# Optimization experiments

Measured on AMD Instinct MI355X. Metric: run time of the kernel, lower is better.

Reference implementation:

```python
import jax, jax.numpy as jnp
import numpy as np

N, F_IN, F_OUT = 8192, 512, 256
ALPHA = 0.2          # LeakyReLU negative slope
NEG_BIG = -9e15      # mask value from the original module


def setup_inputs() -> dict:
    key = jax.random.key(0)
    k1, k2, k3, k4, k5 = jax.random.split(key, 5)
    x = jax.random.normal(k1, (N, F_IN), dtype=jnp.float32)
    adj = jax.random.randint(k2, (N, N), 0, 2, dtype=jnp.int32)
    # xavier_uniform with gain=1.414
    def xavier(k, shape, gain=1.414):
        fan_in, fan_out = shape[0], shape[1]
        bound = gain * np.sqrt(6.0 / (fan_in + fan_out))
        return jax.random.uniform(k, shape, jnp.float32, -bound, bound)
    W = xavier(k3, (F_IN, F_OUT))
    a1 = xavier(k4, (F_OUT, 1))
    a2 = xavier(k5, (F_OUT, 1))
    return {"x": x, "adj": adj, "W": W, "a1": a1, "a2": a2}


def reference(x, adj, W, a1, a2):
    h = x @ W                                   # [N, F_OUT]
    logit_1 = h @ a1                            # [N, 1]
    logit_2 = h @ a2                            # [N, 1]
    e = jax.nn.leaky_relu(logit_1 + logit_2.T, ALPHA)      # [N, N]
    e = jnp.where(adj > 0, e, jnp.float32(NEG_BIG))
    mean_h = jnp.mean(h, axis=0, keepdims=True)            # [1, F_OUT]
    glob_logit = jax.nn.leaky_relu(logit_1 + mean_h @ a2, ALPHA)  # [N, 1]
    e_all = jnp.concatenate([e, glob_logit], axis=-1)      # [N, N+1]
    attention = jax.nn.softmax(e_all, axis=-1)
    h_all = jnp.concatenate([h, mean_h], axis=0)           # [N+1, F_OUT]
    return jax.nn.elu(attention @ h_all)                   # [N, F_OUT]
```

## Files before the change

### kernel.cpp

```cpp
#include <hip/hip_runtime.h>

#define NROW 8192
#define FIN  512
#define FOUT 256
#define ALPHA 0.2f

typedef float  f32x4  __attribute__((ext_vector_type(4)));
typedef int    i32x4  __attribute__((ext_vector_type(4)));
typedef __bf16 bf16x8 __attribute__((ext_vector_type(8)));
typedef __bf16 bf16x4 __attribute__((ext_vector_type(4)));

__device__ __forceinline__ void bar_lds() {
    asm volatile("s_waitcnt lgkmcnt(0)" ::: "memory");
    __builtin_amdgcn_sched_barrier(0);
    __builtin_amdgcn_s_barrier();
}

__global__ void k1_wt(const float* __restrict__ W, unsigned short* __restrict__ WbT_u) {
    __bf16* WbT = (__bf16*)WbT_u;
    __shared__ float tw[32][33];
    int bx = blockIdx.x & 7;
    int by = blockIdx.x >> 3;
    int f0 = bx * 32, k0 = by * 32;
    int tx = threadIdx.x & 31, ty = threadIdx.x >> 5;
#pragma unroll
    for (int r = 0; r < 4; ++r)
        tw[ty + 8*r][tx] = W[(k0 + ty + 8*r) * FOUT + f0 + tx];
    __syncthreads();
#pragma unroll
    for (int r = 0; r < 4; ++r)
        WbT[(f0 + ty + 8*r) * FIN + k0 + tx] = (__bf16)tw[tx][ty + 8*r];
}

__global__ __launch_bounds__(256, 2) void k2_gemm1(const float* __restrict__ x,
                                                   const unsigned short* __restrict__ WbT_u,
                                                   unsigned short* __restrict__ hTb_u) {
    const __bf16* WbT = (const __bf16*)WbT_u;
    __bf16* hTb = (__bf16*)hTb_u;
    int i0 = blockIdx.x * 32;
    int t = threadIdx.x;
    int lane = t & 63, wv = t >> 6;
    int lm = lane & 15, lg = lane >> 4;
    int wf0 = wv * 64;

    f32x4 acc[4][2];
#pragma unroll
    for (int a = 0; a < 4; ++a)
#pragma unroll
        for (int b = 0; b < 2; ++b) acc[a][b] = (f32x4){0.f, 0.f, 0.f, 0.f};

    for (int kt = 0; kt < FIN; kt += 32) {
        bf16x8 af[4];
#pragma unroll
        for (int fi = 0; fi < 4; ++fi)
            af[fi] = *(const bf16x8*)(WbT + (wf0 + fi*16 + lm) * FIN + kt + lg*8);
        bf16x8 bfr[2];
#pragma unroll
        for (int ii = 0; ii < 2; ++ii) {
            const float* xp = x + (i0 + ii*16 + lm) * FIN + kt + lg*8;
            f32x4 v0 = *(const f32x4*)(xp);
            f32x4 v1 = *(const f32x4*)(xp + 4);
            bf16x8 b;
#pragma unroll
            for (int e = 0; e < 4; ++e) { b[e] = (__bf16)v0[e]; b[4+e] = (__bf16)v1[e]; }
            bfr[ii] = b;
        }
#pragma unroll
        for (int fi = 0; fi < 4; ++fi)
#pragma unroll
            for (int ii = 0; ii < 2; ++ii)
                acc[fi][ii] = __builtin_amdgcn_mfma_f32_16x16x32_bf16(af[fi], bfr[ii], acc[fi][ii], 0, 0, 0);
    }
#pragma unroll
    for (int fi = 0; fi < 4; ++fi)
#pragma unroll
        for (int ii = 0; ii < 2; ++ii)
#pragma unroll
            for (int q = 0; q < 4; ++q)
                hTb[(wf0 + fi*16 + lg*4 + q) * NROW + i0 + ii*16 + lm] = (__bf16)acc[fi][ii][q];
}

__global__ void k3_logits(const unsigned short* __restrict__ hTb_u,
                          const float* __restrict__ a1, const float* __restrict__ a2,
                          float* __restrict__ l1, float* __restrict__ l2) {
    const __bf16* hTb = (const __bf16*)hTb_u;
    int i = blockIdx.x * 256 + threadIdx.x;
    float s1 = 0.f, s2 = 0.f;
    for (int f = 0; f < FOUT; ++f) {
        float h = (float)hTb[f * NROW + i];
        s1 += h * a1[f];
        s2 += h * a2[f];
    }
    l1[i] = s1; l2[i] = s2;
}

__global__ void k3_mean(const unsigned short* __restrict__ hTb_u, float* __restrict__ mean_h) {
    const __bf16* hTb = (const __bf16*)hTb_u;
    int f = blockIdx.x;
    int t = threadIdx.x;
    float s = 0.f;
    for (int i = t; i < NROW; i += 256) s += (float)hTb[f * NROW + i];
#pragma unroll
    for (int m = 1; m < 64; m <<= 1) s += __shfl_xor(s, m);
    __shared__ float red[4];
    if ((t & 63) == 0) red[t >> 6] = s;
    __syncthreads();
    if (t == 0) mean_h[f] = (red[0] + red[1] + red[2] + red[3]) * (1.0f / NROW);
}

__global__ __launch_bounds__(256, 2) void k4_attn(const int* __restrict__ adj,
                                                  const unsigned short* __restrict__ hTb_u,
                                                  const float* __restrict__ l1,
                                                  const float* __restrict__ l2,
                                                  float* __restrict__ outpT,
                                                  float* __restrict__ Zp,
                                                  int js, int jwidth, int ntiles) {
    const __bf16* hTb = (const __bf16*)hTb_u;
    __shared__ __align__(16) __bf16 wlds[2][64 * 64];

    int b = blockIdx.x;
    int js_idx = b % js;
    int it = b / js;
    int i0 = it * 64;
    int jstart = js_idx * jwidth;

    int t = threadIdx.x;
    int lane = t & 63, wv = t >> 6;
    int lm = lane & 15, lg = lane >> 4;
    int wf0 = wv * 64;
    int r = t >> 2, cc = t & 3;
    int i_glob = i0 + r;
    float l1v = l1[i_glob];

    const i32x4* adj4 = (const i32x4*)adj;
    const f32x4* l24  = (const f32x4*)l2;
    long arow = (long)i_glob * (NROW / 4);

    f32x4 acc[4][4];
#pragma unroll
    for (int a = 0; a < 4; ++a)
#pragma unroll
        for (int c = 0; c < 4; ++c) acc[a][c] = (f32x4){0.f, 0.f, 0.f, 0.f};
    float zpart = 0.f;

    i32x4 adjA[4], adjB[4];

    auto loadT = [&](i32x4 (&adjR)[4], int jb) {
        int c4 = jb >> 2;
#pragma unroll
        for (int k = 0; k < 4; ++k)
            adjR[k] = adj4[arow + c4 + cc + 4*k];
    };

    auto stageT = [&](int bufi, i32x4 (&adjR)[4], int jb) {
        int c4 = jb >> 2;
        __bf16* wl = wlds[bufi];
        float zadd = 0.f;
#pragma unroll
        for (int k = 0; k < 4; ++k) {
            f32x4 l2v = l24[c4 + cc + 4*k];
            int jl = cc * 4 + 16 * k;
            bf16x4 p;
#pragma unroll
            for (int e = 0; e < 4; ++e) {
                float s = l1v + l2v[e];
                float ex = __expf(fmaxf(s, ALPHA * s));
                float w = (adjR[k][e] > 0) ? ex : 0.0f;
                __bf16 wb = (__bf16)w;
                p[e] = wb;
                zadd += (float)wb;
            }
            int blk = jl >> 3;
            int eo = r * 64 + ((blk ^ (r & 7)) << 3) + (jl & 7);
            *(bf16x4*)(wl + eo) = p;
        }
        zpart += zadd;
    };

    auto mfmaT = [&](int bufi, int jb) {
        const __bf16* wl = wlds[bufi];
        bf16x8 af[2][4];
#pragma unroll
        for (int ks = 0; ks < 2; ++ks)
#pragma unroll
            for (int fi = 0; fi < 4; ++fi)
                af[ks][fi] = *(const bf16x8*)(hTb + (wf0 + fi*16 + lm) * NROW + jb + ks*32 + lg*8);
#pragma unroll
        for (int ks = 0; ks < 2; ++ks) {
            bf16x8 bw[4];
#pragma unroll
            for (int ii = 0; ii < 4; ++ii) {
                int row = ii * 16 + lm;
                int blk = ks * 4 + lg;
                bw[ii] = *(const bf16x8*)(wl + row * 64 + ((blk ^ (row & 7)) << 3));
            }
#pragma unroll
            for (int fi = 0; fi < 4; ++fi)
#pragma unroll
                for (int ii = 0; ii < 4; ++ii)
                    acc[fi][ii] = __builtin_amdgcn_mfma_f32_16x16x32_bf16(af[ks][fi], bw[ii], acc[fi][ii], 0, 0, 0);
        }
    };

    loadT(adjA, jstart);
    stageT(0, adjA, jstart);
    loadT(adjB, jstart + 64);
    bar_lds();
    for (int tt = 0; tt < ntiles; tt += 2) {
        if (tt + 2 < ntiles) loadT(adjA, jstart + (tt + 2) * 64);
        stageT(1, adjB, jstart + (tt + 1) * 64);
        mfmaT(0, jstart + tt * 64);
        bar_lds();
        if (tt + 3 < ntiles) loadT(adjB, jstart + (tt + 3) * 64);
        if (tt + 2 < ntiles) stageT(0, adjA, jstart + (tt + 2) * 64);
        mfmaT(1, jstart + (tt + 1) * 64);
        bar_lds();
    }

    float zs = zpart + __shfl_xor(zpart, 1);
    zs += __shfl_xor(zs, 2);
    if (cc == 0) Zp[js_idx * NROW + i_glob] = zs;

#pragma unroll
    for (int fi = 0; fi < 4; ++fi)
#pragma unroll
        for (int ii = 0; ii < 4; ++ii)
#pragma unroll
            for (int q = 0; q < 4; ++q)
                outpT[(long)js_idx * (NROW * FOUT) + (wf0 + fi*16 + lg*4 + q) * NROW + i0 + ii*16 + lm] = acc[fi][ii][q];
}

__global__ void k5_final(const float* __restrict__ outpT, const float* __restrict__ Zp,
                         const float* __restrict__ l1, const float* __restrict__ mean_h,
                         const float* __restrict__ a2, float* __restrict__ out, int js) {
    __shared__ float tile[64][65];
    __shared__ float red[4];
    __shared__ float s_mda2;
    int b = blockIdx.x;
    int it = b >> 2, ft = b & 3;
    int i0 = it * 64, f0 = ft * 64;
    int t = threadIdx.x;

    float v = mean_h[t] * a2[t];
#pragma unroll
    for (int m = 1; m < 64; m <<= 1) v += __shfl_xor(v, m);
    if ((t & 63) == 0) red[t >> 6] = v;
    __syncthreads();
    if (t == 0) s_mda2 = red[0] + red[1] + red[2] + red[3];

    {
        int fl = t >> 2, icb = (t & 3) * 16;
#pragma unroll
        for (int c = 0; c < 4; ++c) {
            f32x4 vv = (f32x4){0.f, 0.f, 0.f, 0.f};
            for (int s = 0; s < js; ++s) {
                f32x4 u = *(const f32x4*)(outpT + (long)s * (NROW * FOUT) + (f0 + fl) * NROW + i0 + icb + 4*c);
                vv += u;
            }
#pragma unroll
            for (int e = 0; e < 4; ++e) tile[fl][icb + 4*c + e] = vv[e];
        }
    }
    __syncthreads();
    int il = t >> 2, fcb = (t & 3) * 16;
    int i = i0 + il;
    float g = l1[i] + s_mda2;
    float egi = __expf(fmaxf(g, ALPHA * g));
    float z = egi;
    for (int s = 0; s < js; ++s) z += Zp[s * NROW + i];
#pragma unroll
    for (int c = 0; c < 4; ++c) {
        f32x4 o;
#pragma unroll
        for (int e = 0; e < 4; ++e) {
            int fl = fcb + 4*c + e;
            float num = tile[fl][il] + egi * mean_h[f0 + fl];
            float val = num / z;
            o[e] = val > 0.f ? val : (__expf(val) - 1.0f);
        }
        *(f32x4*)(out + (long)i * FOUT + f0 + fcb + 4*c) = o;
    }
}

extern "C" void kernel_launch(void* const* d_in, const int* in_sizes, int n_in,
                              void* d_out, int out_size, void* d_ws, size_t ws_size,
                              hipStream_t stream) {
    const float* x   = (const float*)d_in[0];
    const int*   adj = (const int*)d_in[1];
    const float* W   = (const float*)d_in[2];
    const float* a1  = (const float*)d_in[3];
    const float* a2  = (const float*)d_in[4];
    float* out = (float*)d_out;
    char* ws = (char*)d_ws;

    unsigned short* hTb = (unsigned short*)(ws);
    unsigned short* WbT = (unsigned short*)(ws + 4194304);
    float* l1     = (float*)(ws + 4456448);
    float* l2     = (float*)(ws + 4489216);
    float* mean_h = (float*)(ws + 4521984);
    float* Zp     = (float*)(ws + 4523008);
    float* outpT  = (float*)(ws + 4785152);

    size_t base = 4785152;
    size_t part = (size_t)NROW * FOUT * 4;
    int js = 1;
    if      (ws_size >= base + 4 * part) js = 4;
    else if (ws_size >= base + 2 * part) js = 2;
    int jwidth = NROW / js;
    int ntiles = jwidth / 64;

    hipLaunchKernelGGL(k1_wt,     dim3(128),      dim3(256), 0, stream, W, WbT);
    hipLaunchKernelGGL(k2_gemm1,  dim3(256),      dim3(256), 0, stream, x, WbT, hTb);
    hipLaunchKernelGGL(k3_logits, dim3(32),       dim3(256), 0, stream, hTb, a1, a2, l1, l2);
    hipLaunchKernelGGL(k3_mean,   dim3(256),      dim3(256), 0, stream, hTb, mean_h);
    hipLaunchKernelGGL(k4_attn,   dim3(128 * js), dim3(256), 0, stream, adj, hTb, l1, l2, outpT, Zp, js, jwidth, ntiles);
    hipLaunchKernelGGL(k5_final,  dim3(512),      dim3(256), 0, stream, outpT, Zp, l1, mean_h, a2, out, js);
}
```

Measured before the change: 192.0 us.

## Fuse logit and mean computation into GEMM epilogue; allow 8-way j-split

After: 226.9 us. 1.18x slower.

```diff
diff --git a/kernel.cpp b/kernel.cpp
--- a/kernel.cpp
+++ b/kernel.cpp
@@ -34,7 +34,12 @@
 
 __global__ __launch_bounds__(256, 2) void k2_gemm1(const float* __restrict__ x,
                                                    const unsigned short* __restrict__ WbT_u,
-                                                   unsigned short* __restrict__ hTb_u) {
+                                                   const float* __restrict__ a1,
+                                                   const float* __restrict__ a2,
+                                                   unsigned short* __restrict__ hTb_u,
+                                                   float* __restrict__ l1,
+                                                   float* __restrict__ l2,
+                                                   float* __restrict__ mean_sum) {
     const __bf16* WbT = (const __bf16*)WbT_u;
     __bf16* hTb = (__bf16*)hTb_u;
     int i0 = blockIdx.x * 32;
@@ -71,6 +76,7 @@
             for (int ii = 0; ii < 2; ++ii)
                 acc[fi][ii] = __builtin_amdgcn_mfma_f32_16x16x32_bf16(af[fi], bfr[ii], acc[fi][ii], 0, 0, 0);
     }
+
 #pragma unroll
     for (int fi = 0; fi < 4; ++fi)
 #pragma unroll
@@ -78,34 +84,53 @@
 #pragma unroll
             for (int q = 0; q < 4; ++q)
                 hTb[(wf0 + fi*16 + lg*4 + q) * NROW + i0 + ii*16 + lm] = (__bf16)acc[fi][ii][q];
-}
-
-__global__ void k3_logits(const unsigned short* __restrict__ hTb_u,
-                          const float* __restrict__ a1, const float* __restrict__ a2,
-                          float* __restrict__ l1, float* __restrict__ l2) {
-    const __bf16* hTb = (const __bf16*)hTb_u;
-    int i = blockIdx.x * 256 + threadIdx.x;
-    float s1 = 0.f, s2 = 0.f;
-    for (int f = 0; f < FOUT; ++f) {
-        float h = (float)hTb[f * NROW + i];
-        s1 += h * a1[f];
-        s2 += h * a2[f];
-    }
-    l1[i] = s1; l2[i] = s2;
-}
-
-__global__ void k3_mean(const unsigned short* __restrict__ hTb_u, float* __restrict__ mean_h) {
-    const __bf16* hTb = (const __bf16*)hTb_u;
-    int f = blockIdx.x;
-    int t = threadIdx.x;
-    float s = 0.f;
-    for (int i = t; i < NROW; i += 256) s += (float)hTb[f * NROW + i];
-#pragma unroll
-    for (int m = 1; m < 64; m <<= 1) s += __shfl_xor(s, m);
-    __shared__ float red[4];
-    if ((t & 63) == 0) red[t >> 6] = s;
+
+    float s1[2] = {0.f, 0.f}, s2[2] = {0.f, 0.f};
+    float mh[4][4];
+#pragma unroll
+    for (int fi = 0; fi < 4; ++fi)
+#pragma unroll
+        for (int q = 0; q < 4; ++q) {
+            int f = wf0 + fi*16 + lg*4 + q;
+            float a1v = a1[f], a2v = a2[f];
+            float h0 = acc[fi][0][q], h1 = acc[fi][1][q];
+            s1[0] += h0 * a1v; s1[1] += h1 * a1v;
+            s2[0] += h0 * a2v; s2[1] += h1 * a2v;
+            mh[fi][q] = h0 + h1;
+        }
+#pragma unroll
+    for (int d = 16; d < 64; d <<= 1) {
+        s1[0] += __shfl_xor(s1[0], d); s1[1] += __shfl_xor(s1[1], d);
+        s2[0] += __shfl_xor(s2[0], d); s2[1] += __shfl_xor(s2[1], d);
+    }
+    __shared__ float redA[4][2][16], redB[4][2][16];
+    if (lg == 0) {
+        redA[wv][0][lm] = s1[0]; redA[wv][1][lm] = s1[1];
+        redB[wv][0][lm] = s2[0]; redB[wv][1][lm] = s2[1];
+    }
+#pragma unroll
+    for (int fi = 0; fi < 4; ++fi)
+#pragma unroll
+        for (int q = 0; q < 4; ++q) {
+#pragma unroll
+            for (int d = 1; d < 16; d <<= 1) mh[fi][q] += __shfl_xor(mh[fi][q], d);
+        }
+    if (lm == 0) {
+#pragma unroll
+        for (int fi = 0; fi < 4; ++fi)
+#pragma unroll
+            for (int q = 0; q < 4; ++q)
+                atomicAdd(&mean_sum[wf0 + fi*16 + lg*4 + q], mh[fi][q]);
+    }
     __syncthreads();
-    if (t == 0) mean_h[f] = (red[0] + red[1] + red[2] + red[3]) * (1.0f / NROW);
+    if (t < 32) {
+        int ii = t >> 4, l = t & 15;
+        l1[i0 + ii*16 + l] = redA[0][ii][l] + redA[1][ii][l] + redA[2][ii][l] + redA[3][ii][l];
+    } else if (t < 64) {
+        int tt2 = t - 32;
+        int ii = tt2 >> 4, l = tt2 & 15;
+        l2[i0 + ii*16 + l] = redB[0][ii][l] + redB[1][ii][l] + redB[2][ii][l] + redB[3][ii][l];
+    }
 }
 
 __global__ __launch_bounds__(256, 2) void k4_attn(const int* __restrict__ adj,
@@ -231,17 +256,18 @@
 }
 
 __global__ void k5_final(const float* __restrict__ outpT, const float* __restrict__ Zp,
-                         const float* __restrict__ l1, const float* __restrict__ mean_h,
+                         const float* __restrict__ l1, const float* __restrict__ mean_sum,
                          const float* __restrict__ a2, float* __restrict__ out, int js) {
     __shared__ float tile[64][65];
     __shared__ float red[4];
     __shared__ float s_mda2;
+    const float inv_n = 1.0f / NROW;
     int b = blockIdx.x;
     int it = b >> 2, ft = b & 3;
     int i0 = it * 64, f0 = ft * 64;
     int t = threadIdx.x;
 
-    float v = mean_h[t] * a2[t];
+    float v = mean_sum[t] * inv_n * a2[t];
 #pragma unroll
     for (int m = 1; m < 64; m <<= 1) v += __shfl_xor(v, m);
     if ((t & 63) == 0) red[t >> 6] = v;
@@ -274,7 +300,7 @@
 #pragma unroll
         for (int e = 0; e < 4; ++e) {
             int fl = fcb + 4*c + e;
-            float num = tile[fl][il] + egi * mean_h[f0 + fl];
+            float num = tile[fl][il] + egi * (mean_sum[f0 + fl] * inv_n);
             float val = num / z;
             o[e] = val > 0.f ? val : (__expf(val) - 1.0f);
         }
@@ -295,24 +321,24 @@
 
     unsigned short* hTb = (unsigned short*)(ws);
     unsigned short* WbT = (unsigned short*)(ws + 4194304);
-    float* l1     = (float*)(ws + 4456448);
-    float* l2     = (float*)(ws + 4489216);
-    float* mean_h = (float*)(ws + 4521984);
-    float* Zp     = (float*)(ws + 4523008);
-    float* outpT  = (float*)(ws + 4785152);
+    float* l1       = (float*)(ws + 4456448);
+    float* l2       = (float*)(ws + 4489216);
+    float* mean_sum = (float*)(ws + 4521984);
+    float* Zp       = (float*)(ws + 4523008);
+    float* outpT    = (float*)(ws + 4785152);
 
     size_t base = 4785152;
     size_t part = (size_t)NROW * FOUT * 4;
     int js = 1;
-    if      (ws_size >= base + 4 * part) js = 4;
+    if      (ws_size >= base + 8 * part) js = 8;
+    else if (ws_size >= base + 4 * part) js = 4;
     else if (ws_size >= base + 2 * part) js = 2;
     int jwidth = NROW / js;
     int ntiles = jwidth / 64;
 
+    hipMemsetAsync(mean_sum, 0, FOUT * sizeof(float), stream);
     hipLaunchKernelGGL(k1_wt,     dim3(128),      dim3(256), 0, stream, W, WbT);
-    hipLaunchKernelGGL(k2_gemm1,  dim3(256),      dim3(256), 0, stream, x, WbT, hTb);
-    hipLaunchKernelGGL(k3_logits, dim3(32),       dim3(256), 0, stream, hTb, a1, a2, l1, l2);
-    hipLaunchKernelGGL(k3_mean,   dim3(256),      dim3(256), 0, stream, hTb, mean_h);
+    hipLaunchKernelGGL(k2_gemm1,  dim3(256),      dim3(256), 0, stream, x, WbT, a1, a2, hTb, l1, l2, mean_sum);
     hipLaunchKernelGGL(k4_attn,   dim3(128 * js), dim3(256), 0, stream, adj, hTb, l1, l2, outpT, Zp, js, jwidth, ntiles);
-    hipLaunchKernelGGL(k5_final,  dim3(512),      dim3(256), 0, stream, outpT, Zp, l1, mean_h, a2, out, js);
-}
+    hipLaunchKernelGGL(k5_final,  dim3(512),      dim3(256), 0, stream, outpT, Zp, l1, mean_sum, a2, out, js);
+}
```
